# Performance work log

Measured on AMD Instinct MI355X. Metric: run time of the kernel, lower is better.

## Reference

```python
import jax, jax.numpy as jnp
import numpy as np

# Decode-path (is_prompt=False) flat paged attention, matching
# HPUPagedAttention.forward_decode: batch2block broadcast of queries,
# block-indexed KV gather, per-block QK^T + bias, flat softmax across
# each sequence's blocks (block2batch reductions), then AV.
B = 32        # decode batch size
H = 32        # query heads
H_KV = 8      # kv heads (GQA)
G = H // H_KV # queries per kv head
D = 128       # head size
BS = 128      # cache block size
NB = 16       # blocks per sequence (max ctx 2048)
T = B * NB    # total mapped blocks
N_CACHE = 600 # cache capacity in blocks
SCALE = 1.0 / float(np.sqrt(D))


def setup_inputs() -> dict:
    key = jax.random.key(0)
    ks = jax.random.split(key, 6)
    query = jax.random.normal(ks[0], (B, 1, H * D), jnp.float32)
    new_k = jax.random.normal(ks[1], (B, 1, H_KV * D), jnp.float32)
    new_v = jax.random.normal(ks[2], (B, 1, H_KV * D), jnp.float32)
    key_cache = jax.random.normal(ks[3], (N_CACHE, BS, H_KV, D), jnp.float32)
    value_cache = jax.random.normal(ks[4], (N_CACHE, BS, H_KV, D), jnp.float32)
    block_list = jnp.arange(T, dtype=jnp.int32)            # cache block id per mapped block
    block_groups = jnp.arange(T, dtype=jnp.int32) // NB    # owning sequence per mapped block
    ctx = jax.random.randint(ks[5], (B,), 1024, 2048, jnp.int32)  # ctx len incl. new token
    # the new token is written at position ctx-1 of its sequence
    block_indices = block_list.reshape(B, NB)[jnp.arange(B), (ctx - 1) // BS]
    block_offsets = (ctx - 1) % BS
    pos = (jnp.arange(T) % NB)[:, None] * BS + jnp.arange(BS)[None, :]  # [T, BS] absolute positions
    block_bias = jnp.where(pos < ctx[block_groups][:, None], 0.0, -jnp.inf).astype(jnp.float32)
    return dict(query=query, key=new_k, value=new_v,
                key_cache=key_cache, value_cache=value_cache,
                block_list=block_list, block_groups=block_groups,
                block_indices=block_indices, block_offsets=block_offsets,
                block_bias=block_bias)


def reference(query, key, value, key_cache, value_cache,
              block_list, block_groups, block_indices, block_offsets, block_bias):
    q = query.reshape(B, H, D)
    k_new = key.reshape(B, H_KV, D)
    v_new = value.reshape(B, H_KV, D)
    # VLLMKVCache insert: scatter new decode token into its (block, offset) slot
    key_cache = key_cache.at[block_indices, block_offsets].set(k_new)
    value_cache = value_cache.at[block_indices, block_offsets].set(v_new)
    # batch2block: broadcast each sequence's (scaled) query to all its blocks
    qb = (q * SCALE)[block_groups].reshape(T, H_KV, G, D)
    k = key_cache[block_list]    # [T, BS, H_KV, D] paged gather
    v = value_cache[block_list]  # [T, BS, H_KV, D]
    attn = jnp.einsum('tkgd,tskd->tkgs', qb, k) + block_bias[:, None, None, :]
    # flat softmax across all blocks belonging to the same sequence
    block_max = attn.max(-1)                                             # [T, H_KV, G]
    seg_max = jax.ops.segment_max(block_max, block_groups, num_segments=B)
    p = jnp.exp(attn - seg_max[block_groups][..., None])                 # [T, H_KV, G, BS]
    denom = jax.ops.segment_sum(p.sum(-1), block_groups, num_segments=B)  # [B, H_KV, G]
    o_blk = jnp.einsum('tkgs,tskd->tkgd', p, v)                          # [T, H_KV, G, D]
    o = jax.ops.segment_sum(o_blk, block_groups, num_segments=B)         # block2batch
    return (o / denom[..., None]).reshape(B, 1, H * D)
```

## Files before the change

kernel.cpp:

```cpp
#include <hip/hip_runtime.h>
#include <math.h>

#define B_   32
#define H_   32
#define HKV  8
#define G_   4
#define D_   128
#define BS_  128
#define NB_  16
#define CH_  2
#define NCH  (NB_ / CH_)
#define CP_  (CH_ * BS_)
#define PART_STRIDE (G_ + G_ + G_ * D_)

typedef float v4f __attribute__((ext_vector_type(4)));

__device__ __forceinline__ float dot4(const float4 a, const float4 b) {
    return a.x * b.x + a.y * b.y + a.z * b.z + a.w * b.w;
}

__device__ __forceinline__ float4 ntload4(const float* p) {
    v4f t = __builtin_nontemporal_load((const v4f*)p);
    return make_float4(t.x, t.y, t.z, t.w);
}

__global__ __launch_bounds__(256) void partial_attn(
    const float* __restrict__ query,
    const float* __restrict__ knew,
    const float* __restrict__ vnew,
    const float* __restrict__ kcache,
    const float* __restrict__ vcache,
    const int* __restrict__ block_list,
    const int* __restrict__ bidx, const int* __restrict__ boff,
    float* __restrict__ ws)
{
    __shared__ float q_s[G_][D_];
    __shared__ float sc[CP_][G_];
    __shared__ float red[4][G_];
    __shared__ float mg[G_];
    __shared__ float dn[G_];
    __shared__ float ob[4][G_][D_];

    const int tid  = threadIdx.x;
    const int w    = tid >> 6;
    const int lane = tid & 63;
    const int bx   = blockIdx.x;
    const int ch   = bx & (NCH - 1);
    const int kh   = (bx >> 3) & 7;
    const int b    = bx >> 6;
    constexpr float SCALE = 0.08838834764831845f;

    const int my_bi = bidx[b];
    int jstar = 0;
#pragma unroll
    for (int jj = 0; jj < NB_; ++jj)
        if (block_list[b * NB_ + jj] == my_bi) jstar = jj;
    const int ctx = jstar * BS_ + boff[b] + 1;

    float* wp = ws + (size_t)bx * PART_STRIDE;
    const int chunk_start = ch * CP_;
    if (ctx <= chunk_start) {
        if (tid < 4) wp[tid] = -INFINITY;
        return;
    }

    for (int i = tid; i < G_ * D_; i += 256) {
        const int g = i >> 7, d = i & 127;
        q_s[g][d] = query[(size_t)b * (H_ * D_) + (size_t)(kh * G_ + g) * D_ + d] * SCALE;
    }
    *(float4*)&sc[tid][0] = make_float4(-INFINITY, -INFINITY, -INFINITY, -INFINITY);
    __syncthreads();

    const int jl = w >> 1;
    const int j  = ch * CH_ + jl;
    const int tb = b * NB_ + j;
    const int cb = block_list[tb];
    const int sb_base = (w & 1) * 64;
    const float* kb   = kcache + ((size_t)cb * BS_ * HKV + kh) * D_;
    const float* vb   = vcache + ((size_t)cb * BS_ * HKV + kh) * D_;

    const int wave_start = j * BS_ + sb_base;
    const int valid_rows = min(64, max(0, ctx - wave_start));
    const int newrow = (ctx - 1) - wave_start;
    const float* knew_h = knew + ((size_t)b * HKV + kh) * D_;
    const float* vnew_h = vnew + ((size_t)b * HKV + kh) * D_;

    {
        const int l3 = lane >> 3;
        const int l8 = lane & 7;
        const int doff = l8 * 4;
        const float4 q00 = *(const float4*)&q_s[0][doff];
        const float4 q01 = *(const float4*)&q_s[0][32 + doff];
        const float4 q02 = *(const float4*)&q_s[0][64 + doff];
        const float4 q03 = *(const float4*)&q_s[0][96 + doff];
        const float4 q10 = *(const float4*)&q_s[1][doff];
        const float4 q11 = *(const float4*)&q_s[1][32 + doff];
        const float4 q12 = *(const float4*)&q_s[1][64 + doff];
        const float4 q13 = *(const float4*)&q_s[1][96 + doff];
        const float4 q20 = *(const float4*)&q_s[2][doff];
        const float4 q21 = *(const float4*)&q_s[2][32 + doff];
        const float4 q22 = *(const float4*)&q_s[2][64 + doff];
        const float4 q23 = *(const float4*)&q_s[2][96 + doff];
        const float4 q30 = *(const float4*)&q_s[3][doff];
        const float4 q31 = *(const float4*)&q_s[3][32 + doff];
        const float4 q32 = *(const float4*)&q_s[3][64 + doff];
        const float4 q33 = *(const float4*)&q_s[3][96 + doff];

        const int itA = (valid_rows + 7) >> 3;

        float4 c0 = {0,0,0,0}, c1 = {0,0,0,0}, c2 = {0,0,0,0}, c3 = {0,0,0,0};
        {
            const int r = l3;
            if (r < valid_rows) {
                const float* kr = (r == newrow)
                    ? (knew_h + doff)
                    : (kb + (size_t)(sb_base + r) * (HKV * D_) + doff);
                c0 = ntload4(kr);
                c1 = ntload4(kr + 32);
                c2 = ntload4(kr + 64);
                c3 = ntload4(kr + 96);
            }
        }
        for (int i = 0; i < itA; ++i) {
            float4 n0 = {0,0,0,0}, n1 = {0,0,0,0}, n2 = {0,0,0,0}, n3 = {0,0,0,0};
            const int rn = ((i + 1) << 3) + l3;
            if (rn < valid_rows) {
                const float* kr = (rn == newrow)
                    ? (knew_h + doff)
                    : (kb + (size_t)(sb_base + rn) * (HKV * D_) + doff);
                n0 = ntload4(kr);
                n1 = ntload4(kr + 32);
                n2 = ntload4(kr + 64);
                n3 = ntload4(kr + 96);
            }

            const int r = (i << 3) + l3;
            float d0 = dot4(c0,q00) + dot4(c1,q01) + dot4(c2,q02) + dot4(c3,q03);
            float d1 = dot4(c0,q10) + dot4(c1,q11) + dot4(c2,q12) + dot4(c3,q13);
            float d2 = dot4(c0,q20) + dot4(c1,q21) + dot4(c2,q22) + dot4(c3,q23);
            float d3 = dot4(c0,q30) + dot4(c1,q31) + dot4(c2,q32) + dot4(c3,q33);
#pragma unroll
            for (int m = 4; m >= 1; m >>= 1) {
                d0 += __shfl_xor(d0, m, 64);
                d1 += __shfl_xor(d1, m, 64);
                d2 += __shfl_xor(d2, m, 64);
                d3 += __shfl_xor(d3, m, 64);
            }
            if (l8 == 0 && r < valid_rows) {
                *(float4*)&sc[(w << 6) + r][0] = make_float4(d0, d1, d2, d3);
            }
            c0 = n0; c1 = n1; c2 = n2; c3 = n3;
        }
    }
    __syncthreads();

    {
        const int g = tid & 3;
        const int u = tid >> 2;
        float m = -INFINITY;
#pragma unroll
        for (int i = 0; i < 4; ++i) m = fmaxf(m, sc[u + 64 * i][g]);
#pragma unroll
        for (int msk = 4; msk <= 32; msk <<= 1) m = fmaxf(m, __shfl_xor(m, msk, 64));
        if (lane < 4) red[w][lane] = m;
        __syncthreads();
        if (tid < 4)
            mg[tid] = fmaxf(fmaxf(red[0][tid], red[1][tid]),
                            fmaxf(red[2][tid], red[3][tid]));
        __syncthreads();

        const float gmr = mg[g];
        const float gm  = (gmr == -INFINITY) ? 0.f : gmr;
        float acc = 0.f;
#pragma unroll
        for (int i = 0; i < 4; ++i) {
            const float p = __expf(sc[u + 64 * i][g] - gm);
            sc[u + 64 * i][g] = p;
            acc += p;
        }
#pragma unroll
        for (int msk = 4; msk <= 32; msk <<= 1) acc += __shfl_xor(acc, msk, 64);
        if (lane < 4) red[w][lane] = acc;
        __syncthreads();
        if (tid < 4) dn[tid] = red[0][tid] + red[1][tid] + red[2][tid] + red[3][tid];
        __syncthreads();
    }

    {
        const int half = lane >> 5;
        const int l5   = lane & 31;
        const int dd   = l5 * 4;
        float4 o0 = {0,0,0,0}, o1 = {0,0,0,0}, o2 = {0,0,0,0}, o3 = {0,0,0,0};
        const int itC = min(32, (valid_rows + 1) >> 1);

        float4 cv = {0,0,0,0};
        if (itC > 0) {
            const int r0 = half;
            const float* vr = (r0 == newrow)
                ? (vnew_h + dd)
                : (vb + (size_t)(sb_base + r0) * (HKV * D_) + dd);
            cv = ntload4(vr);
        }
        for (int i = 0; i < itC; ++i) {
            float4 nv = {0,0,0,0};
            if (i + 1 < itC) {
                const int rn = 2 * (i + 1) + half;
                const float* vr = (rn == newrow)
                    ? (vnew_h + dd)
                    : (vb + (size_t)(sb_base + rn) * (HKV * D_) + dd);
                nv = ntload4(vr);
            }
            const int r = 2 * i + half;
            const float4 vv = cv;
            const float4 pp = *(const float4*)&sc[(w << 6) + r][0];
            o0.x += pp.x * vv.x; o0.y += pp.x * vv.y; o0.z += pp.x * vv.z; o0.w += pp.x * vv.w;
            o1.x += pp.y * vv.x; o1.y += pp.y * vv.y; o1.z += pp.y * vv.z; o1.w += pp.y * vv.w;
            o2.x += pp.z * vv.x; o2.y += pp.z * vv.y; o2.z += pp.z * vv.z; o2.w += pp.z * vv.w;
            o3.x += pp.w * vv.x; o3.y += pp.w * vv.y; o3.z += pp.w * vv.z; o3.w += pp.w * vv.w;
            cv = nv;
        }
        o0.x += __shfl_xor(o0.x, 32, 64); o0.y += __shfl_xor(o0.y, 32, 64);
        o0.z += __shfl_xor(o0.z, 32, 64); o0.w += __shfl_xor(o0.w, 32, 64);
        o1.x += __shfl_xor(o1.x, 32, 64); o1.y += __shfl_xor(o1.y, 32, 64);
        o1.z += __shfl_xor(o1.z, 32, 64); o1.w += __shfl_xor(o1.w, 32, 64);
        o2.x += __shfl_xor(o2.x, 32, 64); o2.y += __shfl_xor(o2.y, 32, 64);
        o2.z += __shfl_xor(o2.z, 32, 64); o2.w += __shfl_xor(o2.w, 32, 64);
        o3.x += __shfl_xor(o3.x, 32, 64); o3.y += __shfl_xor(o3.y, 32, 64);
        o3.z += __shfl_xor(o3.z, 32, 64); o3.w += __shfl_xor(o3.w, 32, 64);
        if (half == 0) {
            *(float4*)&ob[w][0][dd] = o0;
            *(float4*)&ob[w][1][dd] = o1;
            *(float4*)&ob[w][2][dd] = o2;
            *(float4*)&ob[w][3][dd] = o3;
        }
    }
    __syncthreads();

    if (tid < 4) { wp[tid] = mg[tid]; wp[4 + tid] = dn[tid]; }
    for (int e = tid; e < G_ * D_; e += 256) {
        const int g = e >> 7, d = e & 127;
        wp[8 + e] = ob[0][g][d] + ob[1][g][d] + ob[2][g][d] + ob[3][g][d];
    }
}

__global__ __launch_bounds__(128) void combine_attn(
    const float* __restrict__ ws, float* __restrict__ out)
{
    const int bk = blockIdx.x;
    const int b  = bk >> 3;
    const int kh = bk & 7;
    const int d  = threadIdx.x;
    const float* base = ws + (size_t)bk * NCH * PART_STRIDE;

#pragma unroll
    for (int g = 0; g < G_; ++g) {
        float M = -INFINITY;
#pragma unroll
        for (int c = 0; c < NCH; ++c)
            M = fmaxf(M, base[c * PART_STRIDE + g]);
        float scales[NCH];
        float L = 0.f;
#pragma unroll
        for (int c = 0; c < NCH; ++c) {
            const float mc = base[c * PART_STRIDE + g];
            const float s  = (mc == -INFINITY) ? 0.f : __expf(mc - M);
            scales[c] = s;
            L += s * base[c * PART_STRIDE + 4 + g];
        }
        float o = 0.f;
#pragma unroll
        for (int c = 0; c < NCH; ++c)
            o += scales[c] * base[c * PART_STRIDE + 8 + g * D_ + d];
        out[(size_t)b * (H_ * D_) + (size_t)(kh * G_ + g) * D_ + d] = o / L;
    }
}

extern "C" void kernel_launch(void* const* d_in, const int* in_sizes, int n_in,
                              void* d_out, int out_size, void* d_ws, size_t ws_size,
                              hipStream_t stream) {
    const float* query = (const float*)d_in[0];
    const float* knew  = (const float*)d_in[1];
    const float* vnew  = (const float*)d_in[2];
    const float* kcache = (const float*)d_in[3];
    const float* vcache = (const float*)d_in[4];
    const int* block_list = (const int*)d_in[5];
    const int* bidx = (const int*)d_in[7];
    const int* boff = (const int*)d_in[8];
    float* out = (float*)d_out;
    float* ws  = (float*)d_ws;

    hipLaunchKernelGGL(partial_attn, dim3(B_ * HKV * NCH), dim3(256), 0, stream,
                       query, knew, vnew, kcache, vcache, block_list,
                       bidx, boff, ws);
    hipLaunchKernelGGL(combine_attn, dim3(B_ * HKV), dim3(128), 0, stream,
                       ws, out);
}
```

Baseline: 555.8 us.

## Make each wave an independent softmax partition and drop block-wide barriers

Each wave now computes its own max, sum and partial output over its 64 rows and writes them directly to a per-wave workspace slot. This removes the shared-memory block-wide reductions, the output staging buffer and most __syncthreads. The query is loaded straight from global into registers, and scores stay in registers until a small per-wave LDS staging step for the AV pass. In exchange the combine kernel must merge 32 partitions instead of 8, which means more workspace traffic, and it guards against NaN from skipped partitions.

After: 593.7 us. 6.8% more time.

```diff
diff --git a/kernel.cpp b/kernel.cpp
--- a/kernel.cpp
+++ b/kernel.cpp
@@ -11,9 +11,12 @@
 #define CH_  2
 #define NCH  (NB_ / CH_)
 #define CP_  (CH_ * BS_)
+#define NPART 32
 #define PART_STRIDE (G_ + G_ + G_ * D_)
 
 typedef float v4f __attribute__((ext_vector_type(4)));
+
+constexpr float SCALE_ = 0.08838834764831845f;
 
 __device__ __forceinline__ float dot4(const float4 a, const float4 b) {
     return a.x * b.x + a.y * b.y + a.z * b.z + a.w * b.w;
@@ -22,6 +25,11 @@
 __device__ __forceinline__ float4 ntload4(const float* p) {
     v4f t = __builtin_nontemporal_load((const v4f*)p);
     return make_float4(t.x, t.y, t.z, t.w);
+}
+
+__device__ __forceinline__ float4 ldq(const float* p) {
+    float4 v = *(const float4*)p;
+    return make_float4(v.x * SCALE_, v.y * SCALE_, v.z * SCALE_, v.w * SCALE_);
 }
 
 __global__ __launch_bounds__(256) void partial_attn(
@@ -34,12 +42,7 @@
     const int* __restrict__ bidx, const int* __restrict__ boff,
     float* __restrict__ ws)
 {
-    __shared__ float q_s[G_][D_];
-    __shared__ float sc[CP_][G_];
-    __shared__ float red[4][G_];
-    __shared__ float mg[G_];
-    __shared__ float dn[G_];
-    __shared__ float ob[4][G_][D_];
+    __shared__ float sc[4][64][G_];
 
     const int tid  = threadIdx.x;
     const int w    = tid >> 6;
@@ -48,7 +51,6 @@
     const int ch   = bx & (NCH - 1);
     const int kh   = (bx >> 3) & 7;
     const int b    = bx >> 6;
-    constexpr float SCALE = 0.08838834764831845f;
 
     const int my_bi = bidx[b];
     int jstar = 0;
@@ -57,150 +59,153 @@
         if (block_list[b * NB_ + jj] == my_bi) jstar = jj;
     const int ctx = jstar * BS_ + boff[b] + 1;
 
-    float* wp = ws + (size_t)bx * PART_STRIDE;
+    float* wp = ws + (size_t)(bx * 4 + w) * PART_STRIDE;
     const int chunk_start = ch * CP_;
     if (ctx <= chunk_start) {
-        if (tid < 4) wp[tid] = -INFINITY;
+        if (lane == 0)
+            *(float4*)wp = make_float4(-INFINITY, -INFINITY, -INFINITY, -INFINITY);
         return;
     }
 
-    for (int i = tid; i < G_ * D_; i += 256) {
-        const int g = i >> 7, d = i & 127;
-        q_s[g][d] = query[(size_t)b * (H_ * D_) + (size_t)(kh * G_ + g) * D_ + d] * SCALE;
-    }
-    *(float4*)&sc[tid][0] = make_float4(-INFINITY, -INFINITY, -INFINITY, -INFINITY);
-    __syncthreads();
-
-    const int jl = w >> 1;
-    const int j  = ch * CH_ + jl;
-    const int tb = b * NB_ + j;
-    const int cb = block_list[tb];
+    const int j  = ch * CH_ + (w >> 1);
+    const int cb = block_list[b * NB_ + j];
     const int sb_base = (w & 1) * 64;
-    const float* kb   = kcache + ((size_t)cb * BS_ * HKV + kh) * D_;
-    const float* vb   = vcache + ((size_t)cb * BS_ * HKV + kh) * D_;
-
+    const float* kb = kcache + ((size_t)cb * BS_ * HKV + kh) * D_;
+    const float* vb = vcache + ((size_t)cb * BS_ * HKV + kh) * D_;
     const int wave_start = j * BS_ + sb_base;
     const int valid_rows = min(64, max(0, ctx - wave_start));
+    if (valid_rows <= 0) {
+        if (lane == 0)
+            *(float4*)wp = make_float4(-INFINITY, -INFINITY, -INFINITY, -INFINITY);
+        return;
+    }
     const int newrow = (ctx - 1) - wave_start;
     const float* knew_h = knew + ((size_t)b * HKV + kh) * D_;
     const float* vnew_h = vnew + ((size_t)b * HKV + kh) * D_;
 
+    const int lr = lane >> 3;
+    const int lc = lane & 7;
+    const int doff = lc * 4;
+
+    const float* qh = query + (size_t)b * (H_ * D_) + (size_t)(kh * G_) * D_;
+    const float4 q00 = ldq(qh + 0*D_ +  0 + doff);
+    const float4 q01 = ldq(qh + 0*D_ + 32 + doff);
+    const float4 q02 = ldq(qh + 0*D_ + 64 + doff);
+    const float4 q03 = ldq(qh + 0*D_ + 96 + doff);
+    const float4 q10 = ldq(qh + 1*D_ +  0 + doff);
+    const float4 q11 = ldq(qh + 1*D_ + 32 + doff);
+    const float4 q12 = ldq(qh + 1*D_ + 64 + doff);
+    const float4 q13 = ldq(qh + 1*D_ + 96 + doff);
+    const float4 q20 = ldq(qh + 2*D_ +  0 + doff);
+    const float4 q21 = ldq(qh + 2*D_ + 32 + doff);
+    const float4 q22 = ldq(qh + 2*D_ + 64 + doff);
+    const float4 q23 = ldq(qh + 2*D_ + 96 + doff);
+    const float4 q30 = ldq(qh + 3*D_ +  0 + doff);
+    const float4 q31 = ldq(qh + 3*D_ + 32 + doff);
+    const float4 q32 = ldq(qh + 3*D_ + 64 + doff);
+    const float4 q33 = ldq(qh + 3*D_ + 96 + doff);
+
+    float4 sreg[8];
+    float4 c0, c1, c2, c3;
     {
-        const int l3 = lane >> 3;
-        const int l8 = lane & 7;
-        const int doff = l8 * 4;
-        const float4 q00 = *(const float4*)&q_s[0][doff];
-        const float4 q01 = *(const float4*)&q_s[0][32 + doff];
-        const float4 q02 = *(const float4*)&q_s[0][64 + doff];
-        const float4 q03 = *(const float4*)&q_s[0][96 + doff];
-        const float4 q10 = *(const float4*)&q_s[1][doff];
-        const float4 q11 = *(const float4*)&q_s[1][32 + doff];
-        const float4 q12 = *(const float4*)&q_s[1][64 + doff];
-        const float4 q13 = *(const float4*)&q_s[1][96 + doff];
-        const float4 q20 = *(const float4*)&q_s[2][doff];
-        const float4 q21 = *(const float4*)&q_s[2][32 + doff];
-        const float4 q22 = *(const float4*)&q_s[2][64 + doff];
-        const float4 q23 = *(const float4*)&q_s[2][96 + doff];
-        const float4 q30 = *(const float4*)&q_s[3][doff];
-        const float4 q31 = *(const float4*)&q_s[3][32 + doff];
-        const float4 q32 = *(const float4*)&q_s[3][64 + doff];
-        const float4 q33 = *(const float4*)&q_s[3][96 + doff];
-
-        const int itA = (valid_rows + 7) >> 3;
-
-        float4 c0 = {0,0,0,0}, c1 = {0,0,0,0}, c2 = {0,0,0,0}, c3 = {0,0,0,0};
-        {
-            const int r = l3;
-            if (r < valid_rows) {
-                const float* kr = (r == newrow)
-                    ? (knew_h + doff)
-                    : (kb + (size_t)(sb_base + r) * (HKV * D_) + doff);
-                c0 = ntload4(kr);
-                c1 = ntload4(kr + 32);
-                c2 = ntload4(kr + 64);
-                c3 = ntload4(kr + 96);
-            }
-        }
-        for (int i = 0; i < itA; ++i) {
-            float4 n0 = {0,0,0,0}, n1 = {0,0,0,0}, n2 = {0,0,0,0}, n3 = {0,0,0,0};
-            const int rn = ((i + 1) << 3) + l3;
-            if (rn < valid_rows) {
-                const float* kr = (rn == newrow)
-                    ? (knew_h + doff)
-                    : (kb + (size_t)(sb_base + rn) * (HKV * D_) + doff);
-                n0 = ntload4(kr);
-                n1 = ntload4(kr + 32);
-                n2 = ntload4(kr + 64);
-                n3 = ntload4(kr + 96);
-            }
-
-            const int r = (i << 3) + l3;
-            float d0 = dot4(c0,q00) + dot4(c1,q01) + dot4(c2,q02) + dot4(c3,q03);
-            float d1 = dot4(c0,q10) + dot4(c1,q11) + dot4(c2,q12) + dot4(c3,q13);
-            float d2 = dot4(c0,q20) + dot4(c1,q21) + dot4(c2,q22) + dot4(c3,q23);
-            float d3 = dot4(c0,q30) + dot4(c1,q31) + dot4(c2,q32) + dot4(c3,q33);
-#pragma unroll
-            for (int m = 4; m >= 1; m >>= 1) {
-                d0 += __shfl_xor(d0, m, 64);
-                d1 += __shfl_xor(d1, m, 64);
-                d2 += __shfl_xor(d2, m, 64);
-                d3 += __shfl_xor(d3, m, 64);
-            }
-            if (l8 == 0 && r < valid_rows) {
-                *(float4*)&sc[(w << 6) + r][0] = make_float4(d0, d1, d2, d3);
-            }
-            c0 = n0; c1 = n1; c2 = n2; c3 = n3;
-        }
-    }
-    __syncthreads();
-
+        const int r = lr;
+        if (r < valid_rows) {
+            const float* kr = (r == newrow)
+                ? (knew_h + doff)
+                : (kb + (size_t)(sb_base + r) * (HKV * D_) + doff);
+            c0 = ntload4(kr);      c1 = ntload4(kr + 32);
+            c2 = ntload4(kr + 64); c3 = ntload4(kr + 96);
+        } else {
+            c0 = c1 = c2 = c3 = make_float4(0, 0, 0, 0);
+        }
+    }
+#pragma unroll
+    for (int i = 0; i < 8; ++i) {
+        float4 n0, n1, n2, n3;
+        n0 = n1 = n2 = n3 = make_float4(0, 0, 0, 0);
+        const int rn = ((i + 1) << 3) + lr;
+        if (rn < valid_rows) {
+            const float* kr = (rn == newrow)
+                ? (knew_h + doff)
+                : (kb + (size_t)(sb_base + rn) * (HKV * D_) + doff);
+            n0 = ntload4(kr);      n1 = ntload4(kr + 32);
+            n2 = ntload4(kr + 64); n3 = ntload4(kr + 96);
+        }
+        float d0 = dot4(c0,q00) + dot4(c1,q01) + dot4(c2,q02) + dot4(c3,q03);
+        float d1 = dot4(c0,q10) + dot4(c1,q11) + dot4(c2,q12) + dot4(c3,q13);
+        float d2 = dot4(c0,q20) + dot4(c1,q21) + dot4(c2,q22) + dot4(c3,q23);
+        float d3 = dot4(c0,q30) + dot4(c1,q31) + dot4(c2,q32) + dot4(c3,q33);
+#pragma unroll
+        for (int msk = 4; msk >= 1; msk >>= 1) {
+            d0 += __shfl_xor(d0, msk, 64);
+            d1 += __shfl_xor(d1, msk, 64);
+            d2 += __shfl_xor(d2, msk, 64);
+            d3 += __shfl_xor(d3, msk, 64);
+        }
+        const bool act = ((i << 3) + lr) < valid_rows;
+        sreg[i] = act ? make_float4(d0, d1, d2, d3)
+                      : make_float4(-INFINITY, -INFINITY, -INFINITY, -INFINITY);
+        c0 = n0; c1 = n1; c2 = n2; c3 = n3;
+    }
+
+    const int half = lane >> 5;
+    const int l5   = lane & 31;
+    const int dd   = l5 * 4;
+    const int itC  = min(32, (valid_rows + 1) >> 1);
+    float4 cv;
     {
-        const int g = tid & 3;
-        const int u = tid >> 2;
-        float m = -INFINITY;
-#pragma unroll
-        for (int i = 0; i < 4; ++i) m = fmaxf(m, sc[u + 64 * i][g]);
-#pragma unroll
-        for (int msk = 4; msk <= 32; msk <<= 1) m = fmaxf(m, __shfl_xor(m, msk, 64));
-        if (lane < 4) red[w][lane] = m;
-        __syncthreads();
-        if (tid < 4)
-            mg[tid] = fmaxf(fmaxf(red[0][tid], red[1][tid]),
-                            fmaxf(red[2][tid], red[3][tid]));
-        __syncthreads();
-
-        const float gmr = mg[g];
-        const float gm  = (gmr == -INFINITY) ? 0.f : gmr;
-        float acc = 0.f;
-#pragma unroll
-        for (int i = 0; i < 4; ++i) {
-            const float p = __expf(sc[u + 64 * i][g] - gm);
-            sc[u + 64 * i][g] = p;
-            acc += p;
-        }
-#pragma unroll
-        for (int msk = 4; msk <= 32; msk <<= 1) acc += __shfl_xor(acc, msk, 64);
-        if (lane < 4) red[w][lane] = acc;
-        __syncthreads();
-        if (tid < 4) dn[tid] = red[0][tid] + red[1][tid] + red[2][tid] + red[3][tid];
-        __syncthreads();
-    }
+        const int r0 = half;
+        const float* vr = (r0 == newrow)
+            ? (vnew_h + dd)
+            : (vb + (size_t)(sb_base + r0) * (HKV * D_) + dd);
+        cv = ntload4(vr);
+    }
+
+    float m0 = -INFINITY, m1 = -INFINITY, m2 = -INFINITY, m3 = -INFINITY;
+#pragma unroll
+    for (int i = 0; i < 8; ++i) {
+        m0 = fmaxf(m0, sreg[i].x); m1 = fmaxf(m1, sreg[i].y);
+        m2 = fmaxf(m2, sreg[i].z); m3 = fmaxf(m3, sreg[i].w);
+    }
+#pragma unroll
+    for (int msk = 8; msk <= 32; msk <<= 1) {
+        m0 = fmaxf(m0, __shfl_xor(m0, msk, 64));
+        m1 = fmaxf(m1, __shfl_xor(m1, msk, 64));
+        m2 = fmaxf(m2, __shfl_xor(m2, msk, 64));
+        m3 = fmaxf(m3, __shfl_xor(m3, msk, 64));
+    }
+    float s0 = 0.f, s1 = 0.f, s2 = 0.f, s3 = 0.f;
+#pragma unroll
+    for (int i = 0; i < 8; ++i) {
+        const float e0 = __expf(sreg[i].x - m0);
+        const float e1 = __expf(sreg[i].y - m1);
+        const float e2 = __expf(sreg[i].z - m2);
+        const float e3 = __expf(sreg[i].w - m3);
+        sreg[i] = make_float4(e0, e1, e2, e3);
+        s0 += e0; s1 += e1; s2 += e2; s3 += e3;
+    }
+#pragma unroll
+    for (int msk = 8; msk <= 32; msk <<= 1) {
+        s0 += __shfl_xor(s0, msk, 64);
+        s1 += __shfl_xor(s1, msk, 64);
+        s2 += __shfl_xor(s2, msk, 64);
+        s3 += __shfl_xor(s3, msk, 64);
+    }
+    if (lane == 0) {
+        *(float4*)(wp)     = make_float4(m0, m1, m2, m3);
+        *(float4*)(wp + 4) = make_float4(s0, s1, s2, s3);
+    }
+
+    if (lc == 0) {
+#pragma unroll
+        for (int i = 0; i < 8; ++i)
+            *(float4*)&sc[w][i * 8 + lr][0] = sreg[i];
+    }
+    asm volatile("s_waitcnt lgkmcnt(0)" ::: "memory");
+    __builtin_amdgcn_sched_barrier(0);
 
     {
-        const int half = lane >> 5;
-        const int l5   = lane & 31;
-        const int dd   = l5 * 4;
         float4 o0 = {0,0,0,0}, o1 = {0,0,0,0}, o2 = {0,0,0,0}, o3 = {0,0,0,0};
-        const int itC = min(32, (valid_rows + 1) >> 1);
-
-        float4 cv = {0,0,0,0};
-        if (itC > 0) {
-            const int r0 = half;
-            const float* vr = (r0 == newrow)
-                ? (vnew_h + dd)
-                : (vb + (size_t)(sb_base + r0) * (HKV * D_) + dd);
-            cv = ntload4(vr);
-        }
         for (int i = 0; i < itC; ++i) {
             float4 nv = {0,0,0,0};
             if (i + 1 < itC) {
@@ -212,7 +217,7 @@
             }
             const int r = 2 * i + half;
             const float4 vv = cv;
-            const float4 pp = *(const float4*)&sc[(w << 6) + r][0];
+            const float4 pp = *(const float4*)&sc[w][r][0];
             o0.x += pp.x * vv.x; o0.y += pp.x * vv.y; o0.z += pp.x * vv.z; o0.w += pp.x * vv.w;
             o1.x += pp.y * vv.x; o1.y += pp.y * vv.y; o1.z += pp.y * vv.z; o1.w += pp.y * vv.w;
             o2.x += pp.z * vv.x; o2.y += pp.z * vv.y; o2.z += pp.z * vv.z; o2.w += pp.z * vv.w;
@@ -228,18 +233,11 @@
         o3.x += __shfl_xor(o3.x, 32, 64); o3.y += __shfl_xor(o3.y, 32, 64);
         o3.z += __shfl_xor(o3.z, 32, 64); o3.w += __shfl_xor(o3.w, 32, 64);
         if (half == 0) {
-            *(float4*)&ob[w][0][dd] = o0;
-            *(float4*)&ob[w][1][dd] = o1;
-            *(float4*)&ob[w][2][dd] = o2;
-            *(float4*)&ob[w][3][dd] = o3;
-        }
-    }
-    __syncthreads();
-
-    if (tid < 4) { wp[tid] = mg[tid]; wp[4 + tid] = dn[tid]; }
-    for (int e = tid; e < G_ * D_; e += 256) {
-        const int g = e >> 7, d = e & 127;
-        wp[8 + e] = ob[0][g][d] + ob[1][g][d] + ob[2][g][d] + ob[3][g][d];
+            *(float4*)(wp + 8 + 0*D_ + dd) = o0;
+            *(float4*)(wp + 8 + 1*D_ + dd) = o1;
+            *(float4*)(wp + 8 + 2*D_ + dd) = o2;
+            *(float4*)(wp + 8 + 3*D_ + dd) = o3;
+        }
     }
 }
 
@@ -250,27 +248,30 @@
     const int b  = bk >> 3;
     const int kh = bk & 7;
     const int d  = threadIdx.x;
-    const float* base = ws + (size_t)bk * NCH * PART_STRIDE;
+    const float* base = ws + (size_t)bk * NPART * PART_STRIDE;
 
 #pragma unroll
     for (int g = 0; g < G_; ++g) {
         float M = -INFINITY;
 #pragma unroll
-        for (int c = 0; c < NCH; ++c)
+        for (int c = 0; c < NPART; ++c)
             M = fmaxf(M, base[c * PART_STRIDE + g]);
-        float scales[NCH];
+        float sarr[NPART];
         float L = 0.f;
 #pragma unroll
-        for (int c = 0; c < NCH; ++c) {
+        for (int c = 0; c < NPART; ++c) {
             const float mc = base[c * PART_STRIDE + g];
             const float s  = (mc == -INFINITY) ? 0.f : __expf(mc - M);
-            scales[c] = s;
-            L += s * base[c * PART_STRIDE + 4 + g];
+            sarr[c] = s;
+            const float lv = base[c * PART_STRIDE + 4 + g];
+            L += (s == 0.f) ? 0.f : s * lv;
         }
         float o = 0.f;
 #pragma unroll
-        for (int c = 0; c < NCH; ++c)
-            o += scales[c] * base[c * PART_STRIDE + 8 + g * D_ + d];
+        for (int c = 0; c < NPART; ++c) {
+            const float ov = base[c * PART_STRIDE + 8 + g * D_ + d];
+            o += (sarr[c] == 0.f) ? 0.f : sarr[c] * ov;
+        }
         out[(size_t)b * (H_ * D_) + (size_t)(kh * G_ + g) * D_ + d] = o / L;
     }
 }
```
